# Kernel tuning notes

Hardware: AMD Instinct MI355X
Metric: run time of the kernel (lower is better)

## Reference

```python
import jax, jax.numpy as jnp
import numpy as np


def setup_inputs() -> dict:
    key = jax.random.key(0)
    k1, k2, k3 = jax.random.split(key, 3)
    B, S, N = 32, 128, 256
    input_real = jax.random.normal(k1, (B, S, N), dtype=jnp.float32)
    input_imag = jax.random.normal(k2, (B, S, N), dtype=jnp.float32)
    weight = jax.random.uniform(k3, (B, S), dtype=jnp.float32)
    return {"input_real": input_real, "input_imag": input_imag, "weight": weight}


def reference(input_real, input_imag, weight):
    # Weighted mixture of rank-1 density matrices over the sequence dim S.
    # output_real[b,n,m] = sum_s w[b,s] * (r[b,s,n]*r[b,s,m] + i[b,s,n]*i[b,s,m])
    # output_imag[b,n,m] = sum_s w[b,s] * (i[b,s,n]*r[b,s,m] - r[b,s,n]*i[b,s,m])
    # Fused: pre-scale one factor by the weight, then a single contraction over S
    # (never materializes the [B,S,N,N] intermediates of the torch code).
    wr = input_real * weight[:, :, None]  # [B,S,N]
    wi = input_imag * weight[:, :, None]  # [B,S,N]
    output_r = jnp.einsum('bsn,bsm->bnm', wr, input_real) + jnp.einsum('bsn,bsm->bnm', wi, input_imag)
    output_i = jnp.einsum('bsn,bsm->bnm', wi, input_real) - jnp.einsum('bsn,bsm->bnm', wr, input_imag)
    return (output_r, output_i)
```

## Files before the change

kernel.cpp:

```cpp
#include <hip/hip_runtime.h>
#include <hip/hip_fp16.h>


constexpr int B = 32, S = 128, N = 256;

typedef _Float16 f16x8 __attribute__((ext_vector_type(8)));
typedef float    f32x4 __attribute__((ext_vector_type(4)));

union F16x8 { f16x8 v; __half2 h2[4]; };

#define MFMA16(a, bv, c) __builtin_amdgcn_mfma_f32_16x16x32_f16((a), (bv), (c), 0, 0, 0)

__global__ __launch_bounds__(512, 4) void ComplexMixture_71313636983193_kernel(
    const float* __restrict__ R, const float* __restrict__ I,
    const float* __restrict__ W, float* __restrict__ Or, float* __restrict__ Oi)
{
    __shared__ alignas(16) _Float16 T[4][64][128];

    const int pb   = blockIdx.x;
    const int lbid = (pb & 7) * 64 + (pb >> 3);
    const int b  = lbid >> 4;
    const int ti = (lbid >> 2) & 3;
    const int tj = lbid & 3;
    const int t  = threadIdx.x;
    const int wv = t >> 6, lane = t & 63;

    const int nquad = t & 15;
    const int octet = (t >> 4) & 7;
    const int side  = (t >> 7) & 1;
    const int arr   = t >> 8;

    const size_t bb = (size_t)b * S * N;
    const int chunk = side ? tj : ti;
    const float* src = (arr ? I : R) + bb + chunk * 64 + nquad * 4;
    const float* Wb  = W + b * S;

    _Float16 (* const Td)[128] = T[side * 2 + arr];

    float4 f0[8];
    #pragma unroll
    for (int s = 0; s < 8; ++s)
        f0[s] = *(const float4*)&src[(size_t)(octet * 8 + s) * N];

    float w0[8], w1[8];
    if (side == 0) {
        const float4 a0 = *(const float4*)&Wb[octet * 8];
        const float4 a1 = *(const float4*)&Wb[octet * 8 + 4];
        const float4 a2 = *(const float4*)&Wb[64 + octet * 8];
        const float4 a3 = *(const float4*)&Wb[64 + octet * 8 + 4];
        w0[0]=a0.x; w0[1]=a0.y; w0[2]=a0.z; w0[3]=a0.w;
        w0[4]=a1.x; w0[5]=a1.y; w0[6]=a1.z; w0[7]=a1.w;
        w1[0]=a2.x; w1[1]=a2.y; w1[2]=a2.z; w1[3]=a2.w;
        w1[4]=a3.x; w1[5]=a3.y; w1[6]=a3.z; w1[7]=a3.w;
    }

    #pragma unroll
    for (int j = 0; j < 4; ++j) {
        const int n    = nquad * 4 + j;
        const int slot = octet ^ ((n >> 1) & 7);
        F16x8 f;
        #pragma unroll
        for (int k = 0; k < 4; ++k) {
            float lo = ((const float*)&f0[2 * k])[j];
            float hi = ((const float*)&f0[2 * k + 1])[j];
            if (side == 0) { lo *= w0[2 * k]; hi *= w0[2 * k + 1]; }
            f.h2[k] = __floats2half2_rn(lo, hi);
        }
        *(f16x8*)&Td[n][slot * 8] = f.v;
    }

    float4 f1[8];
    #pragma unroll
    for (int s = 0; s < 8; ++s)
        f1[s] = *(const float4*)&src[(size_t)(64 + octet * 8 + s) * N];

    __syncthreads();

    const int wn = (wv & 3) * 16;
    const int wm = (wv >> 2) * 32;
    const int fr16 = lane & 15, kb = lane >> 4;
    const int ra  = wn + fr16;          const int sa  = (ra  >> 1) & 7;
    const int rb0 = wm + fr16;          const int sb0 = (rb0 >> 1) & 7;
    const int rb1 = wm + 16 + fr16;     const int sb1 = (rb1 >> 1) & 7;

    f32x4 accR[2] = {}, accA[2] = {}, accB[2] = {};
    f16x8 awr, awi;

#define LOAD_A(ks) { const int ca = (((ks) * 4 + kb) ^ sa) * 8;              \
        awr = *(const f16x8*)&T[0][ra][ca];                                  \
        awi = *(const f16x8*)&T[1][ra][ca]; }
#define STEP_B(ks, ms) { const int K = (ks) * 4 + kb;                        \
        const int rb = (ms) ? rb1 : rb0;                                     \
        const int cb = (K ^ ((ms) ? sb1 : sb0)) * 8;                         \
        const f16x8 br = *(const f16x8*)&T[2][rb][cb];                       \
        const f16x8 bi = *(const f16x8*)&T[3][rb][cb];                       \
        accR[ms] = MFMA16(awr, br, accR[ms]);                                \
        accR[ms] = MFMA16(awi, bi, accR[ms]);                                \
        accA[ms] = MFMA16(awi, br, accA[ms]);                                \
        accB[ms] = MFMA16(awr, bi, accB[ms]); }

    __builtin_amdgcn_s_setprio(1);
    LOAD_A(0); STEP_B(0, 0); STEP_B(0, 1);
    LOAD_A(1); STEP_B(1, 0); STEP_B(1, 1);
    __builtin_amdgcn_s_setprio(0);

    #pragma unroll
    for (int j = 0; j < 4; ++j) {
        const int n    = nquad * 4 + j;
        const int slot = (8 + octet) ^ ((n >> 1) & 7);
        F16x8 f;
        #pragma unroll
        for (int k = 0; k < 4; ++k) {
            float lo = ((const float*)&f1[2 * k])[j];
            float hi = ((const float*)&f1[2 * k + 1])[j];
            if (side == 0) { lo *= w1[2 * k]; hi *= w1[2 * k + 1]; }
            f.h2[k] = __floats2half2_rn(lo, hi);
        }
        *(f16x8*)&Td[n][slot * 8] = f.v;
    }

    __syncthreads();

    const int n0 = ti * 64, m0 = tj * 64;
    const int nn = n0 + wn + kb * 4;

#define STORE_MS(ms) {                                                       \
        const int mm = m0 + wm + (ms) * 16 + fr16;                           \
        _Pragma("unroll")                                                    \
        for (int r = 0; r < 4; ++r) {                                        \
            const size_t o = ((size_t)b * N + nn + r) * N + mm;              \
            Or[o] = accR[ms][r];                                             \
            Oi[o] = accA[ms][r] - accB[ms][r];                               \
        } }

    __builtin_amdgcn_s_setprio(1);
    LOAD_A(2); STEP_B(2, 0); STEP_B(2, 1);
    LOAD_A(3); STEP_B(3, 0);
    __builtin_amdgcn_s_setprio(0);
    STORE_MS(0);
    __builtin_amdgcn_s_setprio(1);
    STEP_B(3, 1);
    __builtin_amdgcn_s_setprio(0);
    STORE_MS(1);
}

extern "C" void kernel_launch(void* const* d_in, const int* in_sizes, int n_in,
                              void* d_out, int out_size, void* d_ws, size_t ws_size,
                              hipStream_t stream) {
    const float* R = (const float*)d_in[0];
    const float* I = (const float*)d_in[1];
    const float* W = (const float*)d_in[2];
    float* Or = (float*)d_out;
    float* Oi = (float*)d_out + (size_t)B * N * N;

    ComplexMixture_71313636983193_kernel<<<dim3(512), dim3(512), 0, stream>>>(
        R, I, W, Or, Oi);
}
```

Baseline: 12.99 us.

## Compute two output tiles per block reusing the A panel across both

Each block now produces two adjacent 64x64 output column tiles that share the same weighted A row panel. The grid is halved to 256 blocks, and shared memory grows to hold A plus two B panels. Each thread loads the full S range per tile instead of splitting S across two stages. The second B panel is loaded and converted while the first tile's MFMAs and stores run. This cuts redundant global reads and fp16 conversion of the A panel, at the cost of fewer blocks, lower occupancy and a longer serial chain per block.

```diff
diff --git a/kernel.cpp b/kernel.cpp
--- a/kernel.cpp
+++ b/kernel.cpp
@@ -11,68 +11,71 @@
 
 #define MFMA16(a, bv, c) __builtin_amdgcn_mfma_f32_16x16x32_f16((a), (bv), (c), 0, 0, 0)
 
-__global__ __launch_bounds__(512, 4) void ComplexMixture_71313636983193_kernel(
+__global__ __launch_bounds__(512, 2) void ComplexMixture_71313636983193_kernel(
     const float* __restrict__ R, const float* __restrict__ I,
     const float* __restrict__ W, float* __restrict__ Or, float* __restrict__ Oi)
 {
-    __shared__ alignas(16) _Float16 T[4][64][128];
+    __shared__ alignas(16) _Float16 T[6][64][128];
 
     const int pb   = blockIdx.x;
-    const int lbid = (pb & 7) * 64 + (pb >> 3);
-    const int b  = lbid >> 4;
-    const int ti = (lbid >> 2) & 3;
-    const int tj = lbid & 3;
+    const int lbid = (pb & 7) * 32 + (pb >> 3);
+    const int b   = lbid >> 3;
+    const int rem = lbid & 7;
+    const int ti  = rem >> 1;
+    const int uu  = rem & 1;
+    const int tj1 = uu * 2, tj2 = uu * 2 + 1;
+
     const int t  = threadIdx.x;
     const int wv = t >> 6, lane = t & 63;
 
     const int nquad = t & 15;
-    const int octet = (t >> 4) & 7;
-    const int side  = (t >> 7) & 1;
+    const int octet = (t >> 4) & 15;
     const int arr   = t >> 8;
+    const int s0    = octet * 8;
 
     const size_t bb = (size_t)b * S * N;
-    const int chunk = side ? tj : ti;
-    const float* src = (arr ? I : R) + bb + chunk * 64 + nquad * 4;
-    const float* Wb  = W + b * S;
+    const float* base  = (arr ? I : R) + bb + nquad * 4;
+    const float* srcA  = base + ti  * 64;
+    const float* srcB1 = base + tj1 * 64;
+    const float* srcB2 = base + tj2 * 64;
+    const float* Wb = W + b * S;
 
-    _Float16 (* const Td)[128] = T[side * 2 + arr];
-
-    float4 f0[8];
+    float4 fA[8], fB1[8];
     #pragma unroll
     for (int s = 0; s < 8; ++s)
-        f0[s] = *(const float4*)&src[(size_t)(octet * 8 + s) * N];
+        fA[s] = *(const float4*)&srcA[(size_t)(s0 + s) * N];
+    #pragma unroll
+    for (int s = 0; s < 8; ++s)
+        fB1[s] = *(const float4*)&srcB1[(size_t)(s0 + s) * N];
 
-    float w0[8], w1[8];
-    if (side == 0) {
-        const float4 a0 = *(const float4*)&Wb[octet * 8];
-        const float4 a1 = *(const float4*)&Wb[octet * 8 + 4];
-        const float4 a2 = *(const float4*)&Wb[64 + octet * 8];
-        const float4 a3 = *(const float4*)&Wb[64 + octet * 8 + 4];
-        w0[0]=a0.x; w0[1]=a0.y; w0[2]=a0.z; w0[3]=a0.w;
-        w0[4]=a1.x; w0[5]=a1.y; w0[6]=a1.z; w0[7]=a1.w;
-        w1[0]=a2.x; w1[1]=a2.y; w1[2]=a2.z; w1[3]=a2.w;
-        w1[4]=a3.x; w1[5]=a3.y; w1[6]=a3.z; w1[7]=a3.w;
+    float w8[8];
+    {
+        const float4 a0 = *(const float4*)&Wb[s0];
+        const float4 a1 = *(const float4*)&Wb[s0 + 4];
+        w8[0]=a0.x; w8[1]=a0.y; w8[2]=a0.z; w8[3]=a0.w;
+        w8[4]=a1.x; w8[5]=a1.y; w8[6]=a1.z; w8[7]=a1.w;
     }
 
     #pragma unroll
     for (int j = 0; j < 4; ++j) {
         const int n    = nquad * 4 + j;
         const int slot = octet ^ ((n >> 1) & 7);
-        F16x8 f;
+        F16x8 fa, fb;
         #pragma unroll
         for (int k = 0; k < 4; ++k) {
-            float lo = ((const float*)&f0[2 * k])[j];
-            float hi = ((const float*)&f0[2 * k + 1])[j];
-            if (side == 0) { lo *= w0[2 * k]; hi *= w0[2 * k + 1]; }
-            f.h2[k] = __floats2half2_rn(lo, hi);
+            fa.h2[k] = __floats2half2_rn(((const float*)&fA[2*k])[j]   * w8[2*k],
+                                         ((const float*)&fA[2*k+1])[j] * w8[2*k+1]);
+            fb.h2[k] = __floats2half2_rn(((const float*)&fB1[2*k])[j],
+                                         ((const float*)&fB1[2*k+1])[j]);
         }
-        *(f16x8*)&Td[n][slot * 8] = f.v;
+        *(f16x8*)&T[arr][n][slot * 8]     = fa.v;
+        *(f16x8*)&T[2 + arr][n][slot * 8] = fb.v;
     }
 
-    float4 f1[8];
+    float4 fB2[8];
     #pragma unroll
     for (int s = 0; s < 8; ++s)
-        f1[s] = *(const float4*)&src[(size_t)(64 + octet * 8 + s) * N];
+        fB2[s] = *(const float4*)&srcB2[(size_t)(s0 + s) * N];
 
     __syncthreads();
 
@@ -83,65 +86,77 @@
     const int rb0 = wm + fr16;          const int sb0 = (rb0 >> 1) & 7;
     const int rb1 = wm + 16 + fr16;     const int sb1 = (rb1 >> 1) & 7;
 
-    f32x4 accR[2] = {}, accA[2] = {}, accB[2] = {};
     f16x8 awr, awi;
 
 #define LOAD_A(ks) { const int ca = (((ks) * 4 + kb) ^ sa) * 8;              \
         awr = *(const f16x8*)&T[0][ra][ca];                                  \
         awi = *(const f16x8*)&T[1][ra][ca]; }
-#define STEP_B(ks, ms) { const int K = (ks) * 4 + kb;                        \
+#define STEP_B(TB, ks, ms, aR, aA, aB) { const int K = (ks) * 4 + kb;        \
         const int rb = (ms) ? rb1 : rb0;                                     \
         const int cb = (K ^ ((ms) ? sb1 : sb0)) * 8;                         \
-        const f16x8 br = *(const f16x8*)&T[2][rb][cb];                       \
-        const f16x8 bi = *(const f16x8*)&T[3][rb][cb];                       \
-        accR[ms] = MFMA16(awr, br, accR[ms]);                                \
-        accR[ms] = MFMA16(awi, bi, accR[ms]);                                \
-        accA[ms] = MFMA16(awi, br, accA[ms]);                                \
-        accB[ms] = MFMA16(awr, bi, accB[ms]); }
+        const f16x8 br = *(const f16x8*)&T[TB][rb][cb];                      \
+        const f16x8 bi = *(const f16x8*)&T[(TB) + 1][rb][cb];                \
+        aR[ms] = MFMA16(awr, br, aR[ms]);                                    \
+        aR[ms] = MFMA16(awi, bi, aR[ms]);                                    \
+        aA[ms] = MFMA16(awi, br, aA[ms]);                                    \
+        aB[ms] = MFMA16(awr, bi, aB[ms]); }
 
-    __builtin_amdgcn_s_setprio(1);
-    LOAD_A(0); STEP_B(0, 0); STEP_B(0, 1);
-    LOAD_A(1); STEP_B(1, 0); STEP_B(1, 1);
-    __builtin_amdgcn_s_setprio(0);
+    const int n0 = ti * 64;
+    const int nn = n0 + wn + kb * 4;
+
+#define STORE_MS(TJ, ms, aR, aA, aB) {                                       \
+        const int mm = (TJ) * 64 + wm + (ms) * 16 + fr16;                    \
+        _Pragma("unroll")                                                    \
+        for (int r = 0; r < 4; ++r) {                                        \
+            const size_t o = ((size_t)b * N + nn + r) * N + mm;              \
+            Or[o] = aR[ms][r];                                               \
+            Oi[o] = aA[ms][r] - aB[ms][r];                                   \
+        } }
+
+    {
+        f32x4 acR[2] = {}, acA[2] = {}, acB[2] = {};
+        __builtin_amdgcn_s_setprio(1);
+        LOAD_A(0); STEP_B(2, 0, 0, acR, acA, acB); STEP_B(2, 0, 1, acR, acA, acB);
+        LOAD_A(1); STEP_B(2, 1, 0, acR, acA, acB); STEP_B(2, 1, 1, acR, acA, acB);
+        LOAD_A(2); STEP_B(2, 2, 0, acR, acA, acB); STEP_B(2, 2, 1, acR, acA, acB);
+        LOAD_A(3); STEP_B(2, 3, 0, acR, acA, acB); STEP_B(2, 3, 1, acR, acA, acB);
+        __builtin_amdgcn_s_setprio(0);
+
+        STORE_MS(tj1, 0, acR, acA, acB);
+        STORE_MS(tj1, 1, acR, acA, acB);
+    }
 
     #pragma unroll
     for (int j = 0; j < 4; ++j) {
         const int n    = nquad * 4 + j;
-        const int slot = (8 + octet) ^ ((n >> 1) & 7);
-        F16x8 f;
+        const int slot = octet ^ ((n >> 1) & 7);
+        F16x8 fb;
         #pragma unroll
-        for (int k = 0; k < 4; ++k) {
-            float lo = ((const float*)&f1[2 * k])[j];
-            float hi = ((const float*)&f1[2 * k + 1])[j];
-            if (side == 0) { lo *= w1[2 * k]; hi *= w1[2 * k + 1]; }
-            f.h2[k] = __floats2half2_rn(lo, hi);
-        }
-        *(f16x8*)&Td[n][slot * 8] = f.v;
+        for (int k = 0; k < 4; ++k)
+            fb.h2[k] = __floats2half2_rn(((const float*)&fB2[2*k])[j],
+                                         ((const float*)&fB2[2*k+1])[j]);
+        *(f16x8*)&T[4 + arr][n][slot * 8] = fb.v;
     }
 
     __syncthreads();
 
-    const int n0 = ti * 64, m0 = tj * 64;
-    const int nn = n0 + wn + kb * 4;
-
-#define STORE_MS(ms) {                                                       \
-        const int mm = m0 + wm + (ms) * 16 + fr16;                           \
-        _Pragma("unroll")                                                    \
-        for (int r = 0; r < 4; ++r) {                                        \
-            const size_t o = ((size_t)b * N + nn + r) * N + mm;              \
-            Or[o] = accR[ms][r];                                             \
-            Oi[o] = accA[ms][r] - accB[ms][r];                               \
-        } }
-
-    __builtin_amdgcn_s_setprio(1);
-    LOAD_A(2); STEP_B(2, 0); STEP_B(2, 1);
-    LOAD_A(3); STEP_B(3, 0);
-    __builtin_amdgcn_s_setprio(0);
-    STORE_MS(0);
-    __builtin_amdgcn_s_setprio(1);
-    STEP_B(3, 1);
-    __builtin_amdgcn_s_setprio(0);
-    STORE_MS(1);
+    {
+        f32x4 acR[2] = {}, acA[2] = {}, acB[2] = {};
+        __builtin_amdgcn_s_setprio(1);
+        LOAD_A(0); STEP_B(4, 0, 0, acR, acA, acB);
+        LOAD_A(1); STEP_B(4, 1, 0, acR, acA, acB);
+        LOAD_A(2); STEP_B(4, 2, 0, acR, acA, acB);
+        LOAD_A(3); STEP_B(4, 3, 0, acR, acA, acB);
+        __builtin_amdgcn_s_setprio(0);
+        STORE_MS(tj2, 0, acR, acA, acB);
+        __builtin_amdgcn_s_setprio(1);
+        LOAD_A(0); STEP_B(4, 0, 1, acR, acA, acB);
+        LOAD_A(1); STEP_B(4, 1, 1, acR, acA, acB);
+        LOAD_A(2); STEP_B(4, 2, 1, acR, acA, acB);
+        LOAD_A(3); STEP_B(4, 3, 1, acR, acA, acB);
+        __builtin_amdgcn_s_setprio(0);
+        STORE_MS(tj2, 1, acR, acA, acB);
+    }
 }
 
 extern "C" void kernel_launch(void* const* d_in, const int* in_sizes, int n_in,
@@ -153,6 +168,6 @@
     float* Or = (float*)d_out;
     float* Oi = (float*)d_out + (size_t)B * N * N;
 
-    ComplexMixture_71313636983193_kernel<<<dim3(512), dim3(512), 0, stream>>>(
+    ComplexMixture_71313636983193_kernel<<<dim3(256), dim3(512), 0, stream>>>(
         R, I, W, Or, Oi);
 }
```

New measurement: 12.84 us. No clear change (-1.2%).

## Enlarge output tile to 128x64 per block to halve redundant input loads

Applied to the files above, without the earlier changes.

Each block now computes a 128x64 output tile instead of 64x64, with 256 blocks instead of 512. Each wave handles two row subtiles, so every loaded B fragment is reused across twice as many MFMAs. The aim is to cut repeated global reads and fp16 conversion of the A-side inputs. In exchange, LDS use per block grows, launch bounds drop to 2 blocks per CU, and only 256 blocks fill the GPU, so occupancy and latency hiding may suffer.

```diff
diff --git a/kernel.cpp b/kernel.cpp
--- a/kernel.cpp
+++ b/kernel.cpp
@@ -11,135 +11,196 @@
 
 #define MFMA16(a, bv, c) __builtin_amdgcn_mfma_f32_16x16x32_f16((a), (bv), (c), 0, 0, 0)
 
-__global__ __launch_bounds__(512, 4) void ComplexMixture_71313636983193_kernel(
+__global__ __launch_bounds__(512, 2) void ComplexMixture_71313636983193_kernel(
     const float* __restrict__ R, const float* __restrict__ I,
     const float* __restrict__ W, float* __restrict__ Or, float* __restrict__ Oi)
 {
-    __shared__ alignas(16) _Float16 T[4][64][128];
+    __shared__ alignas(16) _Float16 AW[2][128][128];
+    __shared__ alignas(16) _Float16 Bt[2][64][128];
 
     const int pb   = blockIdx.x;
-    const int lbid = (pb & 7) * 64 + (pb >> 3);
-    const int b  = lbid >> 4;
-    const int ti = (lbid >> 2) & 3;
-    const int tj = lbid & 3;
+    const int lbid = (pb & 7) * 32 + (pb >> 3);
+    const int b   = lbid >> 3;
+    const int tii = (lbid >> 2) & 1;
+    const int tj  = lbid & 3;
+
     const int t  = threadIdx.x;
     const int wv = t >> 6, lane = t & 63;
 
-    const int nquad = t & 15;
-    const int octet = (t >> 4) & 7;
-    const int side  = (t >> 7) & 1;
-    const int arr   = t >> 8;
+    const bool isA  = (t < 256);
+    const int  u    = t & 255;
+    const int  oct  = (u >> 4) & 7;
+    const int  nqA  = (u & 15) | ((u >> 7) << 4);
+    const int  nqB  = u & 15;
+    const int  arrB = u >> 7;
 
     const size_t bb = (size_t)b * S * N;
-    const int chunk = side ? tj : ti;
-    const float* src = (arr ? I : R) + bb + chunk * 64 + nquad * 4;
-    const float* Wb  = W + b * S;
-
-    _Float16 (* const Td)[128] = T[side * 2 + arr];
-
-    float4 f0[8];
-    #pragma unroll
-    for (int s = 0; s < 8; ++s)
-        f0[s] = *(const float4*)&src[(size_t)(octet * 8 + s) * N];
+    const float* srcAR = R + bb + tii * 128 + nqA * 4;
+    const float* srcAI = I + bb + tii * 128 + nqA * 4;
+    const float* srcB  = (arrB ? I : R) + bb + tj * 64 + nqB * 4;
+    const float* Wb    = W + b * S;
+
+    float4 L0[8], L1[8];
+    if (isA) {
+        #pragma unroll
+        for (int s = 0; s < 8; ++s) {
+            const size_t ro = (size_t)(oct * 8 + s) * N;
+            L0[s] = *(const float4*)&srcAR[ro];
+            L1[s] = *(const float4*)&srcAI[ro];
+        }
+    } else {
+        #pragma unroll
+        for (int s = 0; s < 8; ++s)
+            L0[s] = *(const float4*)&srcB[(size_t)(oct * 8 + s) * N];
+    }
 
     float w0[8], w1[8];
-    if (side == 0) {
-        const float4 a0 = *(const float4*)&Wb[octet * 8];
-        const float4 a1 = *(const float4*)&Wb[octet * 8 + 4];
-        const float4 a2 = *(const float4*)&Wb[64 + octet * 8];
-        const float4 a3 = *(const float4*)&Wb[64 + octet * 8 + 4];
+    if (isA) {
+        const float4 a0 = *(const float4*)&Wb[oct * 8];
+        const float4 a1 = *(const float4*)&Wb[oct * 8 + 4];
+        const float4 a2 = *(const float4*)&Wb[64 + oct * 8];
+        const float4 a3 = *(const float4*)&Wb[64 + oct * 8 + 4];
         w0[0]=a0.x; w0[1]=a0.y; w0[2]=a0.z; w0[3]=a0.w;
         w0[4]=a1.x; w0[5]=a1.y; w0[6]=a1.z; w0[7]=a1.w;
         w1[0]=a2.x; w1[1]=a2.y; w1[2]=a2.z; w1[3]=a2.w;
         w1[4]=a3.x; w1[5]=a3.y; w1[6]=a3.z; w1[7]=a3.w;
     }
 
-    #pragma unroll
-    for (int j = 0; j < 4; ++j) {
-        const int n    = nquad * 4 + j;
-        const int slot = octet ^ ((n >> 1) & 7);
-        F16x8 f;
-        #pragma unroll
-        for (int k = 0; k < 4; ++k) {
-            float lo = ((const float*)&f0[2 * k])[j];
-            float hi = ((const float*)&f0[2 * k + 1])[j];
-            if (side == 0) { lo *= w0[2 * k]; hi *= w0[2 * k + 1]; }
-            f.h2[k] = __floats2half2_rn(lo, hi);
-        }
-        *(f16x8*)&Td[n][slot * 8] = f.v;
-    }
-
-    float4 f1[8];
-    #pragma unroll
-    for (int s = 0; s < 8; ++s)
-        f1[s] = *(const float4*)&src[(size_t)(64 + octet * 8 + s) * N];
+    if (isA) {
+        #pragma unroll
+        for (int j = 0; j < 4; ++j) {
+            const int n    = nqA * 4 + j;
+            const int slot = oct ^ ((n >> 1) & 7);
+            F16x8 fr, fi;
+            #pragma unroll
+            for (int k = 0; k < 4; ++k) {
+                fr.h2[k] = __floats2half2_rn(((const float*)&L0[2*k])[j]   * w0[2*k],
+                                             ((const float*)&L0[2*k+1])[j] * w0[2*k+1]);
+                fi.h2[k] = __floats2half2_rn(((const float*)&L1[2*k])[j]   * w0[2*k],
+                                             ((const float*)&L1[2*k+1])[j] * w0[2*k+1]);
+            }
+            *(f16x8*)&AW[0][n][slot * 8] = fr.v;
+            *(f16x8*)&AW[1][n][slot * 8] = fi.v;
+        }
+    } else {
+        #pragma unroll
+        for (int j = 0; j < 4; ++j) {
+            const int n    = nqB * 4 + j;
+            const int slot = oct ^ ((n >> 1) & 7);
+            F16x8 f;
+            #pragma unroll
+            for (int k = 0; k < 4; ++k)
+                f.h2[k] = __floats2half2_rn(((const float*)&L0[2*k])[j],
+                                            ((const float*)&L0[2*k+1])[j]);
+            *(f16x8*)&Bt[arrB][n][slot * 8] = f.v;
+        }
+    }
+
+    float4 M0[8], M1[8];
+    if (isA) {
+        #pragma unroll
+        for (int s = 0; s < 8; ++s) {
+            const size_t ro = (size_t)(64 + oct * 8 + s) * N;
+            M0[s] = *(const float4*)&srcAR[ro];
+            M1[s] = *(const float4*)&srcAI[ro];
+        }
+    } else {
+        #pragma unroll
+        for (int s = 0; s < 8; ++s)
+            M0[s] = *(const float4*)&srcB[(size_t)(64 + oct * 8 + s) * N];
+    }
 
     __syncthreads();
 
-    const int wn = (wv & 3) * 16;
+    const int wn = (wv & 3) * 32;
     const int wm = (wv >> 2) * 32;
     const int fr16 = lane & 15, kb = lane >> 4;
-    const int ra  = wn + fr16;          const int sa  = (ra  >> 1) & 7;
-    const int rb0 = wm + fr16;          const int sb0 = (rb0 >> 1) & 7;
-    const int rb1 = wm + 16 + fr16;     const int sb1 = (rb1 >> 1) & 7;
-
-    f32x4 accR[2] = {}, accA[2] = {}, accB[2] = {};
-    f16x8 awr, awi;
-
-#define LOAD_A(ks) { const int ca = (((ks) * 4 + kb) ^ sa) * 8;              \
-        awr = *(const f16x8*)&T[0][ra][ca];                                  \
-        awi = *(const f16x8*)&T[1][ra][ca]; }
-#define STEP_B(ks, ms) { const int K = (ks) * 4 + kb;                        \
-        const int rb = (ms) ? rb1 : rb0;                                     \
-        const int cb = (K ^ ((ms) ? sb1 : sb0)) * 8;                         \
-        const f16x8 br = *(const f16x8*)&T[2][rb][cb];                       \
-        const f16x8 bi = *(const f16x8*)&T[3][rb][cb];                       \
-        accR[ms] = MFMA16(awr, br, accR[ms]);                                \
-        accR[ms] = MFMA16(awi, bi, accR[ms]);                                \
-        accA[ms] = MFMA16(awi, br, accA[ms]);                                \
-        accB[ms] = MFMA16(awr, bi, accB[ms]); }
+    const int ra0 = wn + fr16;        const int sa0 = (ra0 >> 1) & 7;
+    const int ra1 = wn + 16 + fr16;   const int sa1 = (ra1 >> 1) & 7;
+    const int rb0 = wm + fr16;        const int sb0 = (rb0 >> 1) & 7;
+    const int rb1 = wm + 16 + fr16;   const int sb1 = (rb1 >> 1) & 7;
+
+    f32x4 accR[2][2] = {}, accA[2][2] = {}, accB[2][2] = {};
+    f16x8 awr[2], awi[2];
+
+#define LOAD_A(ks) { const int K = (ks) * 4 + kb;                            \
+        awr[0] = *(const f16x8*)&AW[0][ra0][(K ^ sa0) * 8];                  \
+        awi[0] = *(const f16x8*)&AW[1][ra0][(K ^ sa0) * 8];                  \
+        awr[1] = *(const f16x8*)&AW[0][ra1][(K ^ sa1) * 8];                  \
+        awi[1] = *(const f16x8*)&AW[1][ra1][(K ^ sa1) * 8]; }
+#define STEP(ks, ms) { const int K = (ks) * 4 + kb;                          \
+        const int rbx = (ms) ? rb1 : rb0;                                    \
+        const int cb  = (K ^ ((ms) ? sb1 : sb0)) * 8;                        \
+        const f16x8 br = *(const f16x8*)&Bt[0][rbx][cb];                     \
+        const f16x8 bi = *(const f16x8*)&Bt[1][rbx][cb];                     \
+        accR[0][ms] = MFMA16(awr[0], br, accR[0][ms]);                       \
+        accR[0][ms] = MFMA16(awi[0], bi, accR[0][ms]);                       \
+        accA[0][ms] = MFMA16(awi[0], br, accA[0][ms]);                       \
+        accB[0][ms] = MFMA16(awr[0], bi, accB[0][ms]);                       \
+        accR[1][ms] = MFMA16(awr[1], br, accR[1][ms]);                       \
+        accR[1][ms] = MFMA16(awi[1], bi, accR[1][ms]);                       \
+        accA[1][ms] = MFMA16(awi[1], br, accA[1][ms]);                       \
+        accB[1][ms] = MFMA16(awr[1], bi, accB[1][ms]); }
 
     __builtin_amdgcn_s_setprio(1);
-    LOAD_A(0); STEP_B(0, 0); STEP_B(0, 1);
-    LOAD_A(1); STEP_B(1, 0); STEP_B(1, 1);
+    LOAD_A(0); STEP(0, 0); STEP(0, 1);
+    LOAD_A(1); STEP(1, 0); STEP(1, 1);
     __builtin_amdgcn_s_setprio(0);
 
-    #pragma unroll
-    for (int j = 0; j < 4; ++j) {
-        const int n    = nquad * 4 + j;
-        const int slot = (8 + octet) ^ ((n >> 1) & 7);
-        F16x8 f;
-        #pragma unroll
-        for (int k = 0; k < 4; ++k) {
-            float lo = ((const float*)&f1[2 * k])[j];
-            float hi = ((const float*)&f1[2 * k + 1])[j];
-            if (side == 0) { lo *= w1[2 * k]; hi *= w1[2 * k + 1]; }
-            f.h2[k] = __floats2half2_rn(lo, hi);
-        }
-        *(f16x8*)&Td[n][slot * 8] = f.v;
+    if (isA) {
+        #pragma unroll
+        for (int j = 0; j < 4; ++j) {
+            const int n    = nqA * 4 + j;
+            const int slot = (8 + oct) ^ ((n >> 1) & 7);
+            F16x8 fr, fi;
+            #pragma unroll
+            for (int k = 0; k < 4; ++k) {
+                fr.h2[k] = __floats2half2_rn(((const float*)&M0[2*k])[j]   * w1[2*k],
+                                             ((const float*)&M0[2*k+1])[j] * w1[2*k+1]);
+                fi.h2[k] = __floats2half2_rn(((const float*)&M1[2*k])[j]   * w1[2*k],
+                                             ((const float*)&M1[2*k+1])[j] * w1[2*k+1]);
+            }
+            *(f16x8*)&AW[0][n][slot * 8] = fr.v;
+            *(f16x8*)&AW[1][n][slot * 8] = fi.v;
+        }
+    } else {
+        #pragma unroll
+        for (int j = 0; j < 4; ++j) {
+            const int n    = nqB * 4 + j;
+            const int slot = (8 + oct) ^ ((n >> 1) & 7);
+            F16x8 f;
+            #pragma unroll
+            for (int k = 0; k < 4; ++k)
+                f.h2[k] = __floats2half2_rn(((const float*)&M0[2*k])[j],
+                                            ((const float*)&M0[2*k+1])[j]);
+            *(f16x8*)&Bt[arrB][n][slot * 8] = f.v;
+        }
     }
 
     __syncthreads();
 
-    const int n0 = ti * 64, m0 = tj * 64;
-    const int nn = n0 + wn + kb * 4;
+    const int nnb = tii * 128 + wn + kb * 4;
 
 #define STORE_MS(ms) {                                                       \
-        const int mm = m0 + wm + (ms) * 16 + fr16;                           \
+        const int mm = tj * 64 + wm + (ms) * 16 + fr16;                      \
         _Pragma("unroll")                                                    \
-        for (int r = 0; r < 4; ++r) {                                        \
-            const size_t o = ((size_t)b * N + nn + r) * N + mm;              \
-            Or[o] = accR[ms][r];                                             \
-            Oi[o] = accA[ms][r] - accB[ms][r];                               \
+        for (int ns = 0; ns < 2; ++ns) {                                     \
+            const int nn = nnb + ns * 16;                                    \
+            _Pragma("unroll")                                                \
+            for (int r = 0; r < 4; ++r) {                                    \
+                const size_t o = ((size_t)b * N + nn + r) * N + mm;          \
+                Or[o] = accR[ns][ms][r];                                     \
+                Oi[o] = accA[ns][ms][r] - accB[ns][ms][r];                   \
+            }                                                                \
         } }
 
     __builtin_amdgcn_s_setprio(1);
-    LOAD_A(2); STEP_B(2, 0); STEP_B(2, 1);
-    LOAD_A(3); STEP_B(3, 0);
+    LOAD_A(2); STEP(2, 0); STEP(2, 1);
+    LOAD_A(3); STEP(3, 0);
     __builtin_amdgcn_s_setprio(0);
     STORE_MS(0);
     __builtin_amdgcn_s_setprio(1);
-    STEP_B(3, 1);
+    STEP(3, 1);
     __builtin_amdgcn_s_setprio(0);
     STORE_MS(1);
 }
@@ -153,6 +214,6 @@
     float* Or = (float*)d_out;
     float* Oi = (float*)d_out + (size_t)B * N * N;
 
-    ComplexMixture_71313636983193_kernel<<<dim3(512), dim3(512), 0, stream>>>(
+    ComplexMixture_71313636983193_kernel<<<dim3(256), dim3(512), 0, stream>>>(
         R, I, W, Or, Oi);
 }
```

Result: slower. 17.53 us (+34.9%).
